# Kernel optimization log

Measured on AMD Instinct MI355X. Metric: run time of the kernel, lower is better.

The kernel has to match this reference:

```python
import jax, jax.numpy as jnp
import numpy as np

N_NODES = 100000
N_EDGES = 1600000
DIMS = [256, 128, 64, 1]  # decoder_dim=256, decoder_l=3 -> 256->128->64->1


def setup_inputs() -> dict:
    key = jax.random.key(0)
    ks = jax.random.split(key, 10)
    inp = {
        "b_z": jax.random.normal(ks[0], (N_NODES, DIMS[0]), jnp.float32),
        "src": jax.random.randint(ks[1], (N_EDGES,), 0, N_NODES, dtype=jnp.int64) if jax.config.jax_enable_x64 else jax.random.randint(ks[1], (N_EDGES,), 0, N_NODES),
        "dst": jax.random.randint(ks[2], (N_EDGES,), 0, N_NODES),
        "b_edge_weight": jax.random.uniform(ks[3], (N_EDGES,), jnp.float32),
        "b_size": 1000,
    }
    for i in range(3):
        inp[f"W{i+1}"] = jax.random.normal(ks[4 + i], (DIMS[i], DIMS[i + 1]), jnp.float32) / np.sqrt(DIMS[i]).astype(np.float32)
        inp[f"b{i+1}"] = jnp.zeros((DIMS[i + 1],), jnp.float32)
    return inp


def _gcn_layer(z, src, dst, ew, W, b, act):
    """DGL GraphConv, norm='both', weight=True, bias=True, in_feats > out_feats."""
    N = z.shape[0]
    ones = jnp.ones(src.shape[0], dtype=z.dtype)
    # unweighted structural degrees, clamped to >= 1 (DGL behavior)
    deg_out = jnp.clip(jax.ops.segment_sum(ones, src, num_segments=N), 1.0)
    deg_in = jnp.clip(jax.ops.segment_sum(ones, dst, num_segments=N), 1.0)
    norm_src = deg_out ** -0.5
    norm_dst = deg_in ** -0.5
    # src-normalize, then project (in > out so weight applied before aggregation)
    h = (z * norm_src[:, None]) @ W          # [N, out]
    m = h[src] * ew[:, None]                 # gather + edge weighting: [E, out]
    rst = jax.ops.segment_sum(m, dst, num_segments=N)  # scatter-sum to dst
    rst = rst * norm_dst[:, None] + b
    return act(rst) if act is not None else rst


def reference(b_z, src, dst, b_edge_weight, b_size, W1, b1, W2, b2, W3, b3):
    z = _gcn_layer(b_z, src, dst, b_edge_weight, W1, b1, jax.nn.relu)
    z = _gcn_layer(z, src, dst, b_edge_weight, W2, b2, jax.nn.relu)
    z = _gcn_layer(z, src, dst, b_edge_weight, W3, b3, None)  # last layer: no activation
    # nonlin_layers is empty (decoder_nonlin_out=None)
    return z.reshape(b_size, -1)
```

## Files before the change

### kernel.cpp

```cpp
#include <hip/hip_runtime.h>


constexpr int D0 = 256, D1 = 128, D2 = 64;
constexpr int NB = 1024;
constexpr int BSH = 7;
constexpr int EBLK = 4096;

typedef __attribute__((ext_vector_type(2))) float f32x2;
typedef __attribute__((ext_vector_type(4))) float f32x4;
typedef __attribute__((ext_vector_type(8))) short short8;

__device__ inline unsigned short f2bf(float f) {
  unsigned u = __builtin_bit_cast(unsigned, f);
  u += 0x7fffu + ((u >> 16) & 1u);
  return (unsigned short)(u >> 16);
}
__device__ inline float bf2f(unsigned short h) {
  unsigned u = ((unsigned)h) << 16;
  return __builtin_bit_cast(float, u);
}
__device__ inline int rdlane_i(int v, int l) { return __builtin_amdgcn_readlane(v, l); }
__device__ inline float rdlane_f(float v, int l) {
  return __builtin_bit_cast(float, __builtin_amdgcn_readlane(__builtin_bit_cast(int, v), l));
}

__global__ void k_chist2(const int* __restrict__ src, const int* __restrict__ dst,
                         int* __restrict__ bc_s, int* __restrict__ bc_d, int E) {
  __shared__ int hs[NB], hd[NB];
  for (int i = threadIdx.x; i < NB; i += 256) { hs[i] = 0; hd[i] = 0; }
  __syncthreads();
  int e0 = blockIdx.x * EBLK, e1 = min(e0 + EBLK, E);
  for (int i = e0 + threadIdx.x; i < e1; i += 256) {
    atomicAdd(&hs[src[i] >> BSH], 1);
    atomicAdd(&hd[dst[i] >> BSH], 1);
  }
  __syncthreads();
  for (int i = threadIdx.x; i < NB; i += 256) {
    bc_s[blockIdx.x * NB + i] = hs[i];
    bc_d[blockIdx.x * NB + i] = hd[i];
  }
}

__global__ void k_binscan(int* __restrict__ bc_s, int* __restrict__ bt_s,
                          int* __restrict__ bc_d, int* __restrict__ bt_d, int nbk) {
  __shared__ int part[16][17];
  int* bc = blockIdx.y ? bc_d : bc_s;
  int* bt = blockIdx.y ? bt_d : bt_s;
  const int j = threadIdx.x & 15;
  const int c = threadIdx.x >> 4;
  const int bin = blockIdx.x * 16 + j;
  const int chunk = (nbk + 15) / 16;
  const int r0 = c * chunk, r1 = min(r0 + chunk, nbk);
  int s = 0;
  for (int b = r0; b < r1; ++b) s += bc[b * NB + bin];
  part[c][j] = s;
  __syncthreads();
  int pre = 0;
  for (int q = 0; q < c; ++q) pre += part[q][j];
  int run = pre;
  for (int b = r0; b < r1; ++b) {
    int v = bc[b * NB + bin];
    bc[b * NB + bin] = run;
    run += v;
  }
  if (c == 15) bt[bin] = run;
}

__global__ void k_btscan(const int* __restrict__ bt_s, int* __restrict__ cbase_s,
                         const int* __restrict__ bt_d, int* __restrict__ cbase_d,
                         int* __restrict__ offs_end, int E) {
  __shared__ int wsum[16];
  const int* bt = blockIdx.x ? bt_d : bt_s;
  int* cbase = blockIdx.x ? cbase_d : cbase_s;
  int tid = threadIdx.x, lane = tid & 63, wid = tid >> 6;
  int v = bt[tid];
  int x = v;
#pragma unroll
  for (int d = 1; d < 64; d <<= 1) { int t = __shfl_up(x, d); if (lane >= d) x += t; }
  if (lane == 63) wsum[wid] = x;
  __syncthreads();
  if (wid == 0 && lane < 16) {
    int s = wsum[lane];
#pragma unroll
    for (int d = 1; d < 16; d <<= 1) { int t = __shfl_up(s, d, 16); if (lane >= d) s += t; }
    wsum[lane] = s;
  }
  __syncthreads();
  int excl = x - v + (wid ? wsum[wid - 1] : 0);
  cbase[tid] = excl;
  if (tid == NB - 1) cbase[NB] = E;
  if (blockIdx.x == 1 && tid == 0) *offs_end = E;
}

__global__ void k_cpart2(const int* __restrict__ src, const int* __restrict__ dst,
                         const float* __restrict__ ew,
                         const int* __restrict__ bc_s, const int* __restrict__ cbase_s,
                         const int* __restrict__ bc_d, const int* __restrict__ cbase_d,
                         int* __restrict__ recs_s, int2* __restrict__ recs_d, int E) {
  __shared__ int cs[NB], cd[NB];
  for (int i = threadIdx.x; i < NB; i += 256) {
    cs[i] = cbase_s[i] + bc_s[blockIdx.x * NB + i];
    cd[i] = cbase_d[i] + bc_d[blockIdx.x * NB + i];
  }
  __syncthreads();
  int e0 = blockIdx.x * EBLK, e1 = min(e0 + EBLK, E);
  for (int i = e0 + threadIdx.x; i < e1; i += 256) {
    int s = src[i], d = dst[i];
    int ps = atomicAdd(&cs[s >> BSH], 1);
    recs_s[ps] = s;
    int pd = atomicAdd(&cd[d >> BSH], 1);
    recs_d[pd] = int2{s | ((d & 127) << 17), __builtin_bit_cast(int, ew[i])};
  }
}

__global__ void k_fine(const int2* __restrict__ recs, const int* __restrict__ cbase,
                       int2* __restrict__ esw, int* __restrict__ offs,
                       float* __restrict__ nd, int N) {
  __shared__ int h[128], cur[128];
  __shared__ int w0tot;
  int bin = blockIdx.x;
  int r0 = cbase[bin], r1 = cbase[bin + 1];
  int t = threadIdx.x;
  if (t < 128) h[t] = 0;
  __syncthreads();
  for (int i = r0 + t; i < r1; i += 256) atomicAdd(&h[recs[i].x >> 17], 1);
  __syncthreads();
  int v = 0, x = 0;
  if (t < 128) {
    v = h[t];
    x = v;
#pragma unroll
    for (int d = 1; d < 64; d <<= 1) { int tt = __shfl_up(x, d); if ((t & 63) >= d) x += tt; }
    if (t == 63) w0tot = x;
  }
  __syncthreads();
  if (t < 128) {
    int excl = x - v + (t >= 64 ? w0tot : 0);
    int node = bin * 128 + t;
    if (node < N) {
      offs[node] = r0 + excl;
      int d = v < 1 ? 1 : v;
      nd[node] = (float)(1.0 / sqrt((double)d));
    }
    cur[t] = r0 + excl;
  }
  __syncthreads();
  for (int i = r0 + t; i < r1; i += 256) {
    int2 rc = recs[i];
    int p = atomicAdd(&cur[rc.x >> 17], 1);
    esw[p] = int2{rc.x & 0x1ffff, rc.y};
  }
}

__global__ void k_fineh(const int* __restrict__ recs, const int* __restrict__ cbase,
                        float* __restrict__ ns, int N) {
  __shared__ int h[128];
  int bin = blockIdx.x;
  int r0 = cbase[bin], r1 = cbase[bin + 1];
  int t = threadIdx.x;
  if (t < 128) h[t] = 0;
  __syncthreads();
  for (int i = r0 + t; i < r1; i += 256) atomicAdd(&h[recs[i] & 127], 1);
  __syncthreads();
  if (t < 128) {
    int node = bin * 128 + t;
    if (node < N) {
      int d = h[t] < 1 ? 1 : h[t];
      ns[node] = (float)(1.0 / sqrt((double)d));
    }
  }
}

__global__ void k_wsplit(const float* __restrict__ W, short* __restrict__ hi,
                         short* __restrict__ lo, int K, int N) {
  int t = blockIdx.x * blockDim.x + threadIdx.x;
  if (t < K * N) {
    int k = t / N, n = t % N;
    float f = W[t];
    unsigned short h = f2bf(f);
    hi[(size_t)n * K + k] = (short)h;
    lo[(size_t)n * K + k] = (short)f2bf(f - bf2f(h));
  }
}

template <int K, int N, int WR, int WC>
__launch_bounds__(256, 2)
__global__ void k_gemm_mfma(const float* __restrict__ A, const float* __restrict__ ns,
                            const short* __restrict__ Wth, const short* __restrict__ Wtl,
                            float* __restrict__ C, int M) {
  constexpr int MR = 128 / WR / 16;
  constexpr int NC = N / WC / 16;
  __shared__ short8 Ah[4 * 128], Al[4 * 128];
  __shared__ short8 Bh[4 * N], Bl[4 * N];
  const int t = threadIdx.x;
  const int block_row = blockIdx.x * 128;
  const int lane = t & 63, wid = t >> 6;
  const int wr = wid / WC, wc = wid % WC;
  const int rowbase = wr * (128 / WR), colbase = wc * (N / WC);
  const int c = lane >> 4, lr = lane & 15;
  f32x4 acc[MR][NC] = {};
  const int r = t & 127;
  const int grow = block_row + r;
  float nsv = 0.f;
  if (t < 128 && grow < M) nsv = ns[grow];

  for (int k0 = 0; k0 < K; k0 += 32) {
    if (t < 128) {
      f32x4 v[8];
      if (grow < M) {
        const f32x4* ap = (const f32x4*)(A + (size_t)grow * K + k0);
#pragma unroll
        for (int i = 0; i < 8; ++i) v[i] = ap[i] * nsv;
      } else {
#pragma unroll
        for (int i = 0; i < 8; ++i) v[i] = f32x4{0.f, 0.f, 0.f, 0.f};
      }
#pragma unroll
      for (int cc = 0; cc < 4; ++cc) {
        short8 hi, lo;
#pragma unroll
        for (int i = 0; i < 8; ++i) {
          float f = v[cc * 2 + (i >> 2)][i & 3];
          unsigned short h = f2bf(f);
          hi[i] = (short)h;
          lo[i] = (short)f2bf(f - bf2f(h));
        }
        Ah[cc * 128 + r] = hi;
        Al[cc * 128 + r] = lo;
      }
    } else {
      const int tt = t - 128;
#pragma unroll
      for (int id = tt; id < N * 4; id += 128) {
        int col = id & (N - 1);
        int cb = id / N;
        Bh[cb * N + col] = *(const short8*)(Wth + (size_t)col * K + k0 + cb * 8);
        Bl[cb * N + col] = *(const short8*)(Wtl + (size_t)col * K + k0 + cb * 8);
      }
    }
    __syncthreads();
    short8 ah[MR], al[MR], bh[NC], bl[NC];
#pragma unroll
    for (int m = 0; m < MR; ++m) {
      int row = rowbase + m * 16 + lr;
      ah[m] = Ah[c * 128 + row];
      al[m] = Al[c * 128 + row];
    }
#pragma unroll
    for (int n = 0; n < NC; ++n) {
      int col = colbase + n * 16 + lr;
      bh[n] = Bh[c * N + col];
      bl[n] = Bl[c * N + col];
    }
#pragma unroll
    for (int m = 0; m < MR; ++m)
#pragma unroll
      for (int n = 0; n < NC; ++n) {
        acc[m][n] = __builtin_amdgcn_mfma_f32_16x16x32_bf16(ah[m], bh[n], acc[m][n], 0, 0, 0);
        acc[m][n] = __builtin_amdgcn_mfma_f32_16x16x32_bf16(ah[m], bl[n], acc[m][n], 0, 0, 0);
        acc[m][n] = __builtin_amdgcn_mfma_f32_16x16x32_bf16(al[m], bh[n], acc[m][n], 0, 0, 0);
      }
    __syncthreads();
  }
#pragma unroll
  for (int m = 0; m < MR; ++m) {
#pragma unroll
    for (int j = 0; j < 4; ++j) {
      int row = block_row + rowbase + m * 16 + (lane >> 4) * 4 + j;
      if (row < M) {
#pragma unroll
        for (int n = 0; n < NC; ++n)
          C[(size_t)row * N + colbase + n * 16 + lr] = acc[m][n][j];
      }
    }
  }
}

__launch_bounds__(256, 4)
__global__ void k_agg128f(const float* __restrict__ h, const int* __restrict__ offs,
                          const int2* __restrict__ esw, const float* __restrict__ nd,
                          const float* __restrict__ b1v, const float* __restrict__ ns,
                          const short* __restrict__ w2h, const short* __restrict__ w2l,
                          float* __restrict__ h2, int M) {
  __shared__ unsigned Ah32[16 * 64], Al32[16 * 64];
  const int t = threadIdx.x, lane = t & 63, wid = t >> 6;
  const int base = blockIdx.x * 16;
  const int nb0 = base + wid * 4;
  const f32x2* hp = (const f32x2*)h;
  f32x2 bv = ((const f32x2*)b1v)[lane];
  int ov = offs[min(nb0 + min(lane, 5), M)];
  int S0[4], S1[4];
#pragma unroll
  for (int q = 0; q < 4; ++q) { S0[q] = rdlane_i(ov, q); S1[q] = rdlane_i(ov, q + 1); }
  int2 ecur{0, 0};
  { int kk = S0[0] + lane; if (kk < S1[0]) ecur = esw[kk]; }
#pragma unroll
  for (int q = 0; q < 4; ++q) {
    const int row = wid * 4 + q;
    const int node = nb0 + q;
    int2 enxt{0, 0};
    if (q < 3) { int kk = S0[q + 1] + lane; if (kk < S1[q + 1]) enxt = esw[kk]; }
    unsigned hi_pack = 0, lo_pack = 0;
    if (node < M) {
      const int s0 = S0[q], s1 = S1[q];
      float a0 = 0.f, a1 = 0.f;
      int2 e = ecur;
      for (int bb = s0; bb < s1; bb += 64) {
        if (bb != s0) { int kk = bb + lane; e = (kk < s1) ? esw[kk] : int2{0, 0}; }
        int sidx = e.x;
        float wt = __builtin_bit_cast(float, e.y);
        int cnt = min(64, s1 - bb);
        for (int jj = 0; jj < cnt; jj += 16) {
          f32x2 v[16];
#pragma unroll
          for (int u = 0; u < 16; ++u) {
            int s = rdlane_i(sidx, jj + u);
            v[u] = hp[(size_t)(unsigned)s * 64 + lane];
          }
          __builtin_amdgcn_sched_barrier(0);
#pragma unroll
          for (int u = 0; u < 16; ++u) {
            float wu = rdlane_f(wt, jj + u);
            a0 += v[u][0] * wu;
            a1 += v[u][1] * wu;
          }
        }
      }
      float ndv = nd[node], nsv = ns[node];
      float z0 = fmaxf(a0 * ndv + bv[0], 0.f) * nsv;
      float z1 = fmaxf(a1 * ndv + bv[1], 0.f) * nsv;
      unsigned short h0 = f2bf(z0), h1b = f2bf(z1);
      hi_pack = (unsigned)h0 | ((unsigned)h1b << 16);
      unsigned short l0 = f2bf(z0 - bf2f(h0)), l1 = f2bf(z1 - bf2f(h1b));
      lo_pack = (unsigned)l0 | ((unsigned)l1 << 16);
    }
    int idx = row * 64 + (lane ^ ((row & 7) << 2));
    Ah32[idx] = hi_pack;
    Al32[idx] = lo_pack;
    ecur = enxt;
  }
  __syncthreads();
  const int colB = wid * 16 + (lane & 15);
  const int koff = (lane >> 4) * 8;
  short8 bh[4], bl[4];
#pragma unroll
  for (int ks = 0; ks < 4; ++ks) {
    bh[ks] = *(const short8*)(w2h + (size_t)colB * 128 + ks * 32 + koff);
    bl[ks] = *(const short8*)(w2l + (size_t)colB * 128 + ks * 32 + koff);
  }
  const int arow = lane & 15, ac = lane >> 4;
  f32x4 acc = {};
#pragma unroll
  for (int ks = 0; ks < 4; ++ks) {
    int bidx = arow * 64 + ((ks * 16 + ac * 4) ^ ((arow & 7) << 2));
    short8 ah = *(const short8*)(Ah32 + bidx);
    short8 al = *(const short8*)(Al32 + bidx);
    acc = __builtin_amdgcn_mfma_f32_16x16x32_bf16(ah, bh[ks], acc, 0, 0, 0);
    acc = __builtin_amdgcn_mfma_f32_16x16x32_bf16(ah, bl[ks], acc, 0, 0, 0);
    acc = __builtin_amdgcn_mfma_f32_16x16x32_bf16(al, bh[ks], acc, 0, 0, 0);
  }
  const int crow = (lane >> 4) * 4;
  const int col = wid * 16 + (lane & 15);
#pragma unroll
  for (int j = 0; j < 4; ++j) {
    int node = base + crow + j;
    if (node < M) h2[(size_t)node * 64 + col] = acc[j];
  }
}

__global__ void k_agg64mv(const float* __restrict__ h, const int* __restrict__ offs,
                          const int2* __restrict__ esw, const float* __restrict__ nd,
                          const float* __restrict__ b2, const float* __restrict__ W3,
                          const float* __restrict__ ns, float* __restrict__ h3, int M) {
  const int lane = threadIdx.x & 63;
  const int wave = blockIdx.x * (blockDim.x >> 6) + (threadIdx.x >> 6);
  const int nb0 = wave * 4;
  if (nb0 >= M) return;
  int ov = offs[min(nb0 + min(lane, 5), M)];
  int S0[4], S1[4];
#pragma unroll
  for (int q = 0; q < 4; ++q) { S0[q] = rdlane_i(ov, q); S1[q] = rdlane_i(ov, q + 1); }
  float bv = b2[lane], w3 = W3[lane];
  int2 ecur{0, 0};
  { int kk = S0[0] + lane; if (kk < S1[0]) ecur = esw[kk]; }
#pragma unroll
  for (int q = 0; q < 4; ++q) {
    const int node = nb0 + q;
    int2 enxt{0, 0};
    if (q < 3) { int kk = S0[q + 1] + lane; if (kk < S1[q + 1]) enxt = esw[kk]; }
    if (node < M) {
      const int s0 = S0[q], s1 = S1[q];
      float acc = 0.f;
      int2 e = ecur;
      for (int bb = s0; bb < s1; bb += 64) {
        if (bb != s0) { int kk = bb + lane; e = (kk < s1) ? esw[kk] : int2{0, 0}; }
        int sidx = e.x;
        float wt = __builtin_bit_cast(float, e.y);
        int cnt = min(64, s1 - bb);
        for (int jj = 0; jj < cnt; jj += 16) {
          float v[16];
#pragma unroll
          for (int u = 0; u < 16; ++u) {
            int s = rdlane_i(sidx, jj + u);
            v[u] = h[(size_t)(unsigned)s * 64 + lane];
          }
          __builtin_amdgcn_sched_barrier(0);
#pragma unroll
          for (int u = 0; u < 16; ++u) acc += v[u] * rdlane_f(wt, jj + u);
        }
      }
      float r = fmaxf(acc * nd[node] + bv, 0.f);
      float p = r * w3;
#pragma unroll
      for (int d = 32; d; d >>= 1) p += __shfl_xor(p, d);
      if (lane == 0) h3[node] = p * ns[node];
    }
    ecur = enxt;
  }
}

__global__ void k_aggfin(const float* __restrict__ h3, const int* __restrict__ offs,
                         const int2* __restrict__ esw, const float* __restrict__ nd,
                         const float* __restrict__ b3, float* __restrict__ out, int M) {
  int i = blockIdx.x * blockDim.x + threadIdx.x;
  if (i >= M) return;
  int s0 = offs[i], s1 = offs[i + 1];
  float acc = 0.f;
  int k = s0;
  for (; k + 4 <= s1; k += 4) {
    int2 e0 = esw[k], e1 = esw[k + 1], e2 = esw[k + 2], e3 = esw[k + 3];
    acc += h3[e0.x] * __builtin_bit_cast(float, e0.y)
         + h3[e1.x] * __builtin_bit_cast(float, e1.y)
         + h3[e2.x] * __builtin_bit_cast(float, e2.y)
         + h3[e3.x] * __builtin_bit_cast(float, e3.y);
  }
  for (; k < s1; ++k) {
    int2 e = esw[k];
    acc += h3[e.x] * __builtin_bit_cast(float, e.y);
  }
  out[i] = acc * nd[i] + b3[0];
}

extern "C" void kernel_launch(void* const* d_in, const int* in_sizes, int n_in,
                              void* d_out, int out_size, void* d_ws, size_t ws_size,
                              hipStream_t stream) {
  const float* b_z = (const float*)d_in[0];
  const int*   src = (const int*)d_in[1];
  const int*   dst = (const int*)d_in[2];
  const float* ew  = (const float*)d_in[3];
  const float* W1  = (const float*)d_in[5];
  const float* b1  = (const float*)d_in[6];
  const float* W2  = (const float*)d_in[7];
  const float* b2  = (const float*)d_in[8];
  const float* W3  = (const float*)d_in[9];
  const float* b3  = (const float*)d_in[10];
  const int N = in_sizes[0] / D0;
  const int E = in_sizes[1];
  float* out = (float*)d_out;

  char* ws = (char*)d_ws;
  size_t off_b = 0;
  auto alloc = [&](size_t bytes) -> void* {
    void* p = ws + off_b;
    off_b += (bytes + 255) & ~(size_t)255;
    return p;
  };
  const int nbk = (E + EBLK - 1) / EBLK;
  int*   bc_s    = (int*)alloc((size_t)nbk * NB * 4);
  int*   bc_d    = (int*)alloc((size_t)nbk * NB * 4);
  int*   bt_s    = (int*)alloc((size_t)NB * 4);
  int*   bt_d    = (int*)alloc((size_t)NB * 4);
  int*   cbase_s = (int*)alloc((size_t)(NB + 1) * 4);
  int*   cbase_d = (int*)alloc((size_t)(NB + 1) * 4);
  int*   offs    = (int*)alloc((size_t)(N + 1) * 4);
  int2*  esw     = (int2*)alloc((size_t)E * 8);
  float* nsrc    = (float*)alloc((size_t)N * 4);
  float* ndst    = (float*)alloc((size_t)N * 4);
  float* h1      = (float*)alloc((size_t)N * D1 * 4);
  float* h2      = (float*)alloc((size_t)N * D2 * 4);
  float* h3      = (float*)alloc((size_t)N * 4);
  short* wt1h    = (short*)alloc((size_t)D0 * D1 * 2);
  short* wt1l    = (short*)alloc((size_t)D0 * D1 * 2);
  short* wt2h    = (short*)alloc((size_t)D1 * D2 * 2);
  short* wt2l    = (short*)alloc((size_t)D1 * D2 * 2);
  int2*  recs_d = (int2*)h1;
  int*   recs_s = (int*)((char*)h1 + ((size_t)16 << 20));

  k_chist2<<<nbk, 256, 0, stream>>>(src, dst, bc_s, bc_d, E);
  k_binscan<<<dim3(NB / 16, 2), 256, 0, stream>>>(bc_s, bt_s, bc_d, bt_d, nbk);
  k_btscan<<<2, 1024, 0, stream>>>(bt_s, cbase_s, bt_d, cbase_d, &offs[N], E);
  k_cpart2<<<nbk, 256, 0, stream>>>(src, dst, ew, bc_s, cbase_s, bc_d, cbase_d,
                                    recs_s, recs_d, E);
  k_fineh<<<NB, 256, 0, stream>>>(recs_s, cbase_s, nsrc, N);
  k_fine<<<NB, 256, 0, stream>>>(recs_d, cbase_d, esw, offs, ndst, N);

  k_wsplit<<<(D0 * D1 + 255) / 256, 256, 0, stream>>>(W1, wt1h, wt1l, D0, D1);
  k_wsplit<<<(D1 * D2 + 255) / 256, 256, 0, stream>>>(W2, wt2h, wt2l, D1, D2);

  k_gemm_mfma<D0, D1, 2, 2><<<(N + 127) / 128, 256, 0, stream>>>(b_z, nsrc, wt1h, wt1l, h1, N);
  k_agg128f<<<(N + 15) / 16, 256, 0, stream>>>(h1, offs, esw, ndst, b1, nsrc,
                                               wt2h, wt2l, h2, N);
  k_agg64mv<<<(N + 15) / 16, 256, 0, stream>>>(h2, offs, esw, ndst, b2, W3, nsrc, h3, N);
  k_aggfin<<<(N + 255) / 256, 256, 0, stream>>>(h3, offs, esw, ndst, b3, out, N);
}
```

Before: 328.3 us.

## Widen aggregation gathers to 16-byte loads and merge setup kernels

The 128-wide and 64-wide aggregation kernels now split each wave so that half-waves (or quarter-waves) each gather a different edge's row using f32x4 loads. The partial sums are combined afterwards with cross-lane shuffles. This is meant to raise bytes per load instruction and halve the number of gather loop iterations. Separately, the fine-binning kernels for src and dst degrees are fused into one launch, and the two weight-split kernels are merged into one, to cut launch overhead. The cost is extra readlane/select work and shuffle reductions, and the fused fine kernel serialises work that used to run as two launches.

```diff
diff --git a/kernel.cpp b/kernel.cpp
--- a/kernel.cpp
+++ b/kernel.cpp
@@ -113,17 +113,18 @@
   }
 }
 
-__global__ void k_fine(const int2* __restrict__ recs, const int* __restrict__ cbase,
-                       int2* __restrict__ esw, int* __restrict__ offs,
-                       float* __restrict__ nd, int N) {
+__global__ void k_finecomb(const int2* __restrict__ recs_d, const int* __restrict__ cbase_d,
+                           const int* __restrict__ recs_s, const int* __restrict__ cbase_s,
+                           int2* __restrict__ esw, int* __restrict__ offs,
+                           float* __restrict__ nd, float* __restrict__ ns, int N) {
   __shared__ int h[128], cur[128];
   __shared__ int w0tot;
   int bin = blockIdx.x;
-  int r0 = cbase[bin], r1 = cbase[bin + 1];
+  int r0 = cbase_d[bin], r1 = cbase_d[bin + 1];
   int t = threadIdx.x;
   if (t < 128) h[t] = 0;
   __syncthreads();
-  for (int i = r0 + t; i < r1; i += 256) atomicAdd(&h[recs[i].x >> 17], 1);
+  for (int i = r0 + t; i < r1; i += 256) atomicAdd(&h[recs_d[i].x >> 17], 1);
   __syncthreads();
   int v = 0, x = 0;
   if (t < 128) {
@@ -146,21 +147,15 @@
   }
   __syncthreads();
   for (int i = r0 + t; i < r1; i += 256) {
-    int2 rc = recs[i];
+    int2 rc = recs_d[i];
     int p = atomicAdd(&cur[rc.x >> 17], 1);
     esw[p] = int2{rc.x & 0x1ffff, rc.y};
   }
-}
-
-__global__ void k_fineh(const int* __restrict__ recs, const int* __restrict__ cbase,
-                        float* __restrict__ ns, int N) {
-  __shared__ int h[128];
-  int bin = blockIdx.x;
-  int r0 = cbase[bin], r1 = cbase[bin + 1];
-  int t = threadIdx.x;
+  __syncthreads();
   if (t < 128) h[t] = 0;
   __syncthreads();
-  for (int i = r0 + t; i < r1; i += 256) atomicAdd(&h[recs[i] & 127], 1);
+  int s0 = cbase_s[bin], s1 = cbase_s[bin + 1];
+  for (int i = s0 + t; i < s1; i += 256) atomicAdd(&h[recs_s[i] & 127], 1);
   __syncthreads();
   if (t < 128) {
     int node = bin * 128 + t;
@@ -171,15 +166,23 @@
   }
 }
 
-__global__ void k_wsplit(const float* __restrict__ W, short* __restrict__ hi,
-                         short* __restrict__ lo, int K, int N) {
+__global__ void k_wsplit2(const float* __restrict__ W1, short* __restrict__ w1h,
+                          short* __restrict__ w1l, const float* __restrict__ W2,
+                          short* __restrict__ w2h, short* __restrict__ w2l) {
   int t = blockIdx.x * blockDim.x + threadIdx.x;
-  if (t < K * N) {
-    int k = t / N, n = t % N;
-    float f = W[t];
+  if (t < D0 * D1) {
+    int k = t / D1, n = t % D1;
+    float f = W1[t];
     unsigned short h = f2bf(f);
-    hi[(size_t)n * K + k] = (short)h;
-    lo[(size_t)n * K + k] = (short)f2bf(f - bf2f(h));
+    w1h[(size_t)n * D0 + k] = (short)h;
+    w1l[(size_t)n * D0 + k] = (short)f2bf(f - bf2f(h));
+  } else if (t < D0 * D1 + D1 * D2) {
+    int i = t - D0 * D1;
+    int k = i / D2, n = i % D2;
+    float f = W2[i];
+    unsigned short h = f2bf(f);
+    w2h[(size_t)n * D1 + k] = (short)h;
+    w2l[(size_t)n * D1 + k] = (short)f2bf(f - bf2f(h));
   }
 }
 
@@ -286,8 +289,10 @@
   const int t = threadIdx.x, lane = t & 63, wid = t >> 6;
   const int base = blockIdx.x * 16;
   const int nb0 = base + wid * 4;
-  const f32x2* hp = (const f32x2*)h;
-  f32x2 bv = ((const f32x2*)b1v)[lane];
+  const f32x4* hp4 = (const f32x4*)h;
+  const int p = lane & 31;
+  const int hi = lane >> 5;
+  f32x4 bv = ((const f32x4*)b1v)[p];
   int ov = offs[min(nb0 + min(lane, 5), M)];
   int S0[4], S1[4];
 #pragma unroll
@@ -300,10 +305,10 @@
     const int node = nb0 + q;
     int2 enxt{0, 0};
     if (q < 3) { int kk = S0[q + 1] + lane; if (kk < S1[q + 1]) enxt = esw[kk]; }
-    unsigned hi_pack = 0, lo_pack = 0;
+    unsigned hw0 = 0, hw1 = 0, lw0 = 0, lw1 = 0;
     if (node < M) {
       const int s0 = S0[q], s1 = S1[q];
-      float a0 = 0.f, a1 = 0.f;
+      f32x4 acc = {};
       int2 e = ecur;
       for (int bb = s0; bb < s1; bb += 64) {
         if (bb != s0) { int kk = bb + lane; e = (kk < s1) ? esw[kk] : int2{0, 0}; }
@@ -311,32 +316,45 @@
         float wt = __builtin_bit_cast(float, e.y);
         int cnt = min(64, s1 - bb);
         for (int jj = 0; jj < cnt; jj += 16) {
-          f32x2 v[16];
-#pragma unroll
-          for (int u = 0; u < 16; ++u) {
-            int s = rdlane_i(sidx, jj + u);
-            v[u] = hp[(size_t)(unsigned)s * 64 + lane];
+          f32x4 v[8];
+#pragma unroll
+          for (int u = 0; u < 8; ++u) {
+            int r0 = rdlane_i(sidx, jj + 2 * u);
+            int r1 = rdlane_i(sidx, jj + 2 * u + 1);
+            int s = hi ? r1 : r0;
+            v[u] = hp4[(size_t)(unsigned)s * 32 + p];
           }
           __builtin_amdgcn_sched_barrier(0);
 #pragma unroll
-          for (int u = 0; u < 16; ++u) {
-            float wu = rdlane_f(wt, jj + u);
-            a0 += v[u][0] * wu;
-            a1 += v[u][1] * wu;
+          for (int u = 0; u < 8; ++u) {
+            float w0 = rdlane_f(wt, jj + 2 * u);
+            float w1 = rdlane_f(wt, jj + 2 * u + 1);
+            float wu = hi ? w1 : w0;
+            acc[0] += v[u][0] * wu;
+            acc[1] += v[u][1] * wu;
+            acc[2] += v[u][2] * wu;
+            acc[3] += v[u][3] * wu;
           }
         }
       }
+      f32x4 o;
+#pragma unroll
+      for (int i = 0; i < 4; ++i) o[i] = acc[i] + __shfl_xor(acc[i], 32);
       float ndv = nd[node], nsv = ns[node];
-      float z0 = fmaxf(a0 * ndv + bv[0], 0.f) * nsv;
-      float z1 = fmaxf(a1 * ndv + bv[1], 0.f) * nsv;
-      unsigned short h0 = f2bf(z0), h1b = f2bf(z1);
-      hi_pack = (unsigned)h0 | ((unsigned)h1b << 16);
-      unsigned short l0 = f2bf(z0 - bf2f(h0)), l1 = f2bf(z1 - bf2f(h1b));
-      lo_pack = (unsigned)l0 | ((unsigned)l1 << 16);
-    }
-    int idx = row * 64 + (lane ^ ((row & 7) << 2));
-    Ah32[idx] = hi_pack;
-    Al32[idx] = lo_pack;
+      float z[4];
+#pragma unroll
+      for (int i = 0; i < 4; ++i) z[i] = fmaxf(o[i] * ndv + bv[i], 0.f) * nsv;
+      unsigned short h0 = f2bf(z[0]), h1b = f2bf(z[1]), h2b = f2bf(z[2]), h3b = f2bf(z[3]);
+      hw0 = (unsigned)h0 | ((unsigned)h1b << 16);
+      hw1 = (unsigned)h2b | ((unsigned)h3b << 16);
+      lw0 = (unsigned)f2bf(z[0] - bf2f(h0)) | ((unsigned)f2bf(z[1] - bf2f(h1b)) << 16);
+      lw1 = (unsigned)f2bf(z[2] - bf2f(h2b)) | ((unsigned)f2bf(z[3] - bf2f(h3b)) << 16);
+    }
+    if (lane < 32) {
+      int widx = (2 * p) ^ ((row & 7) << 2);
+      *(uint2*)&Ah32[row * 64 + widx] = uint2{hw0, hw1};
+      *(uint2*)&Al32[row * 64 + widx] = uint2{lw0, lw1};
+    }
     ecur = enxt;
   }
   __syncthreads();
@@ -376,11 +394,16 @@
   const int wave = blockIdx.x * (blockDim.x >> 6) + (threadIdx.x >> 6);
   const int nb0 = wave * 4;
   if (nb0 >= M) return;
+  const f32x4* hp4 = (const f32x4*)h;
+  const int p = lane & 15;
+  const int q4 = lane >> 4;
+  const bool qb0 = q4 & 1, qb1 = q4 & 2;
+  f32x4 bv = ((const f32x4*)b2)[p];
+  f32x4 w3v = ((const f32x4*)W3)[p];
   int ov = offs[min(nb0 + min(lane, 5), M)];
   int S0[4], S1[4];
 #pragma unroll
   for (int q = 0; q < 4; ++q) { S0[q] = rdlane_i(ov, q); S1[q] = rdlane_i(ov, q + 1); }
-  float bv = b2[lane], w3 = W3[lane];
   int2 ecur{0, 0};
   { int kk = S0[0] + lane; if (kk < S1[0]) ecur = esw[kk]; }
 #pragma unroll
@@ -390,30 +413,53 @@
     if (q < 3) { int kk = S0[q + 1] + lane; if (kk < S1[q + 1]) enxt = esw[kk]; }
     if (node < M) {
       const int s0 = S0[q], s1 = S1[q];
-      float acc = 0.f;
+      f32x4 acc = {};
       int2 e = ecur;
       for (int bb = s0; bb < s1; bb += 64) {
         if (bb != s0) { int kk = bb + lane; e = (kk < s1) ? esw[kk] : int2{0, 0}; }
         int sidx = e.x;
         float wt = __builtin_bit_cast(float, e.y);
         int cnt = min(64, s1 - bb);
-        for (int jj = 0; jj < cnt; jj += 16) {
-          float v[16];
-#pragma unroll
-          for (int u = 0; u < 16; ++u) {
-            int s = rdlane_i(sidx, jj + u);
-            v[u] = h[(size_t)(unsigned)s * 64 + lane];
+        for (int jj = 0; jj < cnt; jj += 32) {
+          f32x4 v[8];
+#pragma unroll
+          for (int u = 0; u < 8; ++u) {
+            int ei = jj + 4 * u;
+            int r0 = rdlane_i(sidx, ei), r1 = rdlane_i(sidx, ei + 1);
+            int r2 = rdlane_i(sidx, ei + 2), r3 = rdlane_i(sidx, ei + 3);
+            int c01 = qb0 ? r1 : r0;
+            int c23 = qb0 ? r3 : r2;
+            int s = qb1 ? c23 : c01;
+            v[u] = hp4[(size_t)(unsigned)s * 16 + p];
           }
           __builtin_amdgcn_sched_barrier(0);
 #pragma unroll
-          for (int u = 0; u < 16; ++u) acc += v[u] * rdlane_f(wt, jj + u);
+          for (int u = 0; u < 8; ++u) {
+            int ei = jj + 4 * u;
+            float w0 = rdlane_f(wt, ei), w1 = rdlane_f(wt, ei + 1);
+            float w2 = rdlane_f(wt, ei + 2), w3s = rdlane_f(wt, ei + 3);
+            float c01 = qb0 ? w1 : w0;
+            float c23 = qb0 ? w3s : w2;
+            float wu = qb1 ? c23 : c01;
+            acc[0] += v[u][0] * wu;
+            acc[1] += v[u][1] * wu;
+            acc[2] += v[u][2] * wu;
+            acc[3] += v[u][3] * wu;
+          }
         }
       }
-      float r = fmaxf(acc * nd[node] + bv, 0.f);
-      float p = r * w3;
-#pragma unroll
-      for (int d = 32; d; d >>= 1) p += __shfl_xor(p, d);
-      if (lane == 0) h3[node] = p * ns[node];
+#pragma unroll
+      for (int i = 0; i < 4; ++i) {
+        acc[i] += __shfl_xor(acc[i], 16);
+        acc[i] += __shfl_xor(acc[i], 32);
+      }
+      float ndv = nd[node];
+      float dp = 0.f;
+#pragma unroll
+      for (int i = 0; i < 4; ++i) dp += fmaxf(acc[i] * ndv + bv[i], 0.f) * w3v[i];
+#pragma unroll
+      for (int d = 8; d; d >>= 1) dp += __shfl_xor(dp, d);
+      if (lane == 0) h3[node] = dp * ns[node];
     }
     ecur = enxt;
   }
@@ -491,11 +537,10 @@
   k_btscan<<<2, 1024, 0, stream>>>(bt_s, cbase_s, bt_d, cbase_d, &offs[N], E);
   k_cpart2<<<nbk, 256, 0, stream>>>(src, dst, ew, bc_s, cbase_s, bc_d, cbase_d,
                                     recs_s, recs_d, E);
-  k_fineh<<<NB, 256, 0, stream>>>(recs_s, cbase_s, nsrc, N);
-  k_fine<<<NB, 256, 0, stream>>>(recs_d, cbase_d, esw, offs, ndst, N);
-
-  k_wsplit<<<(D0 * D1 + 255) / 256, 256, 0, stream>>>(W1, wt1h, wt1l, D0, D1);
-  k_wsplit<<<(D1 * D2 + 255) / 256, 256, 0, stream>>>(W2, wt2h, wt2l, D1, D2);
+  k_finecomb<<<NB, 256, 0, stream>>>(recs_d, cbase_d, recs_s, cbase_s, esw, offs,
+                                     ndst, nsrc, N);
+  k_wsplit2<<<(D0 * D1 + D1 * D2 + 255) / 256, 256, 0, stream>>>(W1, wt1h, wt1l,
+                                                                 W2, wt2h, wt2l);
 
   k_gemm_mfma<D0, D1, 2, 2><<<(N + 127) / 128, 256, 0, stream>>>(b_z, nsrc, wt1h, wt1l, h1, N);
   k_agg128f<<<(N + 15) / 16, 256, 0, stream>>>(h1, offs, esw, ndst, b1, nsrc,
```

New measurement: 323.8 us. No clear change (-1.4%).
